# Kernel optimization log

Hardware: AMD Instinct MI355X
Metric: run time of the kernel (lower is better)

## Reference

```python
import jax, jax.numpy as jnp
import numpy as np

NEG_INF = -1e10
LEAKY_ALPHA = 0.2


def setup_inputs() -> dict:
    key = jax.random.key(0)
    k1, k2, k3, k4, k5 = jax.random.split(key, 5)
    N, F, H, D = 4096, 512, 8, 64
    X = jax.random.normal(k1, (N, F), dtype=jnp.float32)
    # dense 0/1 adjacency (float, as used by the mask formula)
    A = jax.random.randint(k2, (N, N), 0, 2).astype(jnp.float32)
    W = jax.random.normal(k3, (H, F, D), dtype=jnp.float32) * (1.0 / np.sqrt(F))
    b = jnp.zeros((H, D), dtype=jnp.float32)
    a_self = jax.random.normal(k4, (H, D), dtype=jnp.float32) * (1.0 / np.sqrt(D))
    a_neigh = jax.random.normal(k5, (H, D), dtype=jnp.float32) * (1.0 / np.sqrt(D))
    return {"X": X, "A": A, "W": W, "b": b, "a_self": a_self, "a_neigh": a_neigh}


def reference(X, A, W, b, a_self, a_neigh):
    # Multi-head dense GAT, heads vectorized. Dropout is identity (eval mode).
    # feats: [H, N, D]
    feats = jnp.einsum('nf,hfd->hnd', X, W)
    e_self = jnp.einsum('hnd,hd->hn', feats, a_self)    # [H, N]
    e_neigh = jnp.einsum('hnd,hd->hn', feats, a_neigh)  # [H, N]
    # outer-sum additive scores: [H, N, N]
    dense = e_self[:, :, None] + e_neigh[:, None, :]
    dense = jnp.where(dense >= 0, dense, LEAKY_ALPHA * dense)  # LeakyReLU(0.2)
    mask = NEG_INF * (1.0 - A)                                  # [N, N]
    dense = dense + mask[None, :, :]
    attn = jax.nn.softmax(dense, axis=-1)                       # [H, N, N]
    out = jnp.einsum('hnm,hmd->hnd', attn, feats) + b[:, None, :]
    # concat heads -> [N, H*D], then relu activation
    H, N, D = out.shape
    out = jnp.transpose(out, (1, 0, 2)).reshape(N, H * D)
    return jax.nn.relu(out)
```

## Files before the change

### kernel.cpp

```cpp
#include <hip/hip_runtime.h>
#include <hip/hip_fp16.h>
#include <stdint.h>


#define NODES 4096
#define FEAT  512
#define HEADS 8
#define DH    64
#define NT    (NODES / 64)

using half2v = __attribute__((ext_vector_type(2))) _Float16;
using half8  = __attribute__((ext_vector_type(8))) _Float16;
using f32x4  = __attribute__((ext_vector_type(4))) float;

__device__ __forceinline__ void gll16(const void* g, void* l) {
    __builtin_amdgcn_global_load_lds(
        (const __attribute__((address_space(1))) uint32_t*)g,
        (__attribute__((address_space(3))) uint32_t*)l, 16, 0, 0);
}

__device__ __forceinline__ uint32_t fenc(float f) {
    uint32_t u = __float_as_uint(f);
    return (u >> 31) ? ~u : (u | 0x80000000u);
}
__device__ __forceinline__ float fdec(uint32_t e) {
    uint32_t u = (e >> 31) ? (e & 0x7FFFFFFFu) : ~e;
    return __uint_as_float(u);
}

#define PACK_BLOCKS 16384
#define CAST_BLOCKS (NODES * FEAT / 4 / 256)
#define WT_BLOCKS   (HEADS * 8)

__global__ __launch_bounds__(256) void prep_kernel(
    const float* __restrict__ A, const float* __restrict__ X, const float* __restrict__ W,
    uint64_t* __restrict__ AbitsT, _Float16* __restrict__ Xh, _Float16* __restrict__ WT,
    uint32_t* __restrict__ enmax_u) {
    __shared__ float t[64][65];
    const int bx = blockIdx.x;
    if (bx < PACK_BLOCKS) {
        const int w    = threadIdx.x >> 6;
        const int lane = threadIdx.x & 63;
        const int v    = bx * 4 + w;
        const int wc   = v >> 10;
        const int rowb = (v & 1023) * 4;
        const float* ar = A + (size_t)wc * 64 + lane;
#pragma unroll
        for (int tt = 0; tt < 4; ++tt) {
            uint64_t m = __ballot(ar[(size_t)(rowb + tt) * NODES] != 0.0f);
            if (lane == 0) AbitsT[(size_t)wc * NODES + rowb + tt] = m;
        }
        return;
    }
    if (bx < PACK_BLOCKS + CAST_BLOCKS) {
        if (bx == PACK_BLOCKS && threadIdx.x < 16) enmax_u[threadIdx.x] = 0;
        int i = ((bx - PACK_BLOCKS) * 256 + threadIdx.x) * 4;
        f32x4 x = *(const f32x4*)(X + i);
        *(half2v*)(Xh + i)     = half2v{(_Float16)x[0], (_Float16)x[1]};
        *(half2v*)(Xh + i + 2) = half2v{(_Float16)x[2], (_Float16)x[3]};
        return;
    }
    const int b2 = bx - PACK_BLOCKS - CAST_BLOCKS;
    const int h  = b2 >> 3;
    const int ft = b2 & 7;
    const int r  = threadIdx.x >> 6;
    const int c  = threadIdx.x & 63;
#pragma unroll
    for (int r0 = 0; r0 < 64; r0 += 4)
        t[r0 + r][c] = W[((size_t)h * FEAT + ft * 64 + r0 + r) * DH + c];
    __syncthreads();
#pragma unroll
    for (int r0 = 0; r0 < 64; r0 += 4)
        WT[((size_t)h * DH + r0 + r) * FEAT + ft * 64 + c] = (_Float16)t[c][r0 + r];
}

__global__ __launch_bounds__(256) void feats_kernel(
    const _Float16* __restrict__ Xh, const _Float16* __restrict__ WT,
    const float* __restrict__ a_self, const float* __restrict__ a_neigh,
    _Float16* __restrict__ Vt, float* __restrict__ e_self,
    _Float16* __restrict__ u_tab, _Float16* __restrict__ v_tab,
    uint32_t* __restrict__ enmax_u) {
    const int h    = blockIdx.y;
    const int bx   = blockIdx.x;
    const int tid  = threadIdx.x;
    const int w    = tid >> 6;
    const int lane = tid & 63;
    const int l15  = lane & 15;
    const int g    = lane >> 4;
    const int n0   = bx * 64 + w * 16;

    f32x4 acc[4] = {};
    const _Float16* xb = Xh + (n0 + l15) * FEAT + g * 8;
    const _Float16* wb = WT + (h * DH + l15) * FEAT + g * 8;

#pragma unroll
    for (int kk = 0; kk < FEAT / 32; ++kk) {
        half8 b = *(const half8*)(xb + kk * 32);
#pragma unroll
        for (int mi = 0; mi < 4; ++mi) {
            half8 a = *(const half8*)(wb + mi * 16 * FEAT + kk * 32);
            acc[mi] = __builtin_amdgcn_mfma_f32_16x16x32_f16(a, b, acc[mi], 0, 0, 0);
        }
    }

    const int cc = w * 2 + (l15 >> 3);
    const int e  = l15 & 7;
    float ps = 0.f, pn = 0.f;
#pragma unroll
    for (int mi = 0; mi < 4; ++mi) {
#pragma unroll
        for (int r = 0; r < 4; ++r) {
            int d = mi * 16 + g * 4 + r;
            float v = acc[mi][r];
            Vt[((size_t)h * NT + bx) * 4096 + cc * 512 + d * 8 + e] = (_Float16)v;
            ps += v * a_self[h * DH + d];
            pn += v * a_neigh[h * DH + d];
        }
    }
    ps += __shfl_xor(ps, 16); ps += __shfl_xor(ps, 32);
    pn += __shfl_xor(pn, 16); pn += __shfl_xor(pn, 32);
    if (g == 0) {
        int n = n0 + l15;
        e_self[h * NODES + n] = ps;
        u_tab[h * NODES + n]  = (_Float16)__expf(pn);
        v_tab[h * NODES + n]  = (_Float16)__expf(0.2f * pn);
    }
    float mx = pn;
    mx = fmaxf(mx, __shfl_xor(mx, 1));
    mx = fmaxf(mx, __shfl_xor(mx, 2));
    mx = fmaxf(mx, __shfl_xor(mx, 4));
    mx = fmaxf(mx, __shfl_xor(mx, 8));
    if (lane == 0) atomicMax(enmax_u + h, fenc(mx));
}

__global__ __launch_bounds__(256, 4) void attn_kernel(
    const uint64_t* __restrict__ AbitsT, const _Float16* __restrict__ Vt,
    const float* __restrict__ e_self, const _Float16* __restrict__ u_tab,
    const _Float16* __restrict__ v_tab, const uint32_t* __restrict__ enmax_u,
    const float* __restrict__ bias, float* __restrict__ out) {
    __shared__ __align__(16) _Float16 Vlds[2][2][4096];
    float* redf = (float*)&Vlds[0][0][0];

    const int tid  = threadIdx.x;
    const int w    = tid >> 6;
    const int lane = tid & 63;
    const int l15  = lane & 15;
    const int g    = lane >> 4;
    const int g8   = g * 8;
    const int rh   = w & 1;
    const int jq   = w >> 1;
    const int h    = blockIdx.x & 7;
    const int i0   = (blockIdx.x >> 3) * 32;

    const float em = fdec(enmax_u[h]);
    const float es = e_self[h * NODES + i0 + rh * 16 + l15];
    const float t0 = es + em;
    const float M  = fmaxf(t0, 0.2f * t0);
    const _Float16 c1 = (_Float16)__expf(es - M);
    const _Float16 c2 = (_Float16)__expf(0.2f * es - M);
    const half2v c1h = half2v{c1, c1};
    const half2v c2h = half2v{c2, c2};

    const _Float16* ub  = u_tab + h * NODES + jq * 2048 + g8;
    const _Float16* vb  = v_tab + h * NODES + jq * 2048 + g8;
    const uint64_t* ab  = AbitsT + (size_t)(jq * 32) * NODES + i0 + rh * 16 + l15;
    const _Float16* vtb = Vt + ((size_t)h * NT + jq * 32) * 4096;

#define STAGE(s_, buf_) do {                                        \
        const _Float16* vs_ = vtb + (size_t)(s_) * 4096;            \
        _Float16* vd_ = &Vlds[jq][buf_][0];                         \
        _Pragma("unroll")                                           \
        for (int p_ = 0; p_ < 4; ++p_) {                            \
            const int c_ = rh * 256 + p_ * 64 + lane;               \
            gll16(vs_ + c_ * 8, vd_ + c_ * 8);                      \
        }                                                           \
    } while (0)

    f32x4 acc[4] = {};
    f32x4 asum = {};
    half8 ones;
#pragma unroll
    for (int e = 0; e < 8; ++e) ones[e] = (_Float16)1.0f;

    STAGE(0, 0);
    uint64_t wb_c = ab[0];
    half8 uf_c[2], vf_c[2];
#pragma unroll
    for (int kk = 0; kk < 2; ++kk) {
        uf_c[kk] = *(const half8*)(ub + kk * 32);
        vf_c[kk] = *(const half8*)(vb + kk * 32);
    }
    __syncthreads();

    for (int s = 0; s < 32; ++s) {
        const int buf = s & 1;
        STAGE(s + 1, buf ^ 1);
        uint64_t wb_n = ab[(size_t)(s + 1) * NODES];
        half8 uf_n[2], vf_n[2];
#pragma unroll
        for (int kk = 0; kk < 2; ++kk) {
            uf_n[kk] = *(const half8*)(ub + (s + 1) * 64 + kk * 32);
            vf_n[kk] = *(const half8*)(vb + (s + 1) * 64 + kk * 32);
        }

        const _Float16* vl = &Vlds[jq][buf][0];
#pragma unroll
        for (int kk = 0; kk < 2; ++kk) {
            const uint32_t b0 = ((uint32_t)(wb_c >> (kk * 32)) >> g8) & 0xFFu;
            half8 paf;
#pragma unroll
            for (int q = 0; q < 4; ++q) {
                half2v u2 = half2v{uf_c[kk][2 * q], uf_c[kk][2 * q + 1]};
                half2v v2 = half2v{vf_c[kk][2 * q], vf_c[kk][2 * q + 1]};
                half2v p2 = __builtin_elementwise_max(u2 * c1h, v2 * c2h);
                uint32_t mlo = (uint32_t)(-(int32_t)((b0 >> (2 * q)) & 1u));
                uint32_t mhi = (uint32_t)(-(int32_t)((b0 >> (2 * q + 1)) & 1u));
                uint32_t m = (mhi & 0xFFFF0000u) | (mlo & 0xFFFFu);
                p2 = __builtin_bit_cast(half2v, __builtin_bit_cast(uint32_t, p2) & m);
                paf[2 * q] = p2[0]; paf[2 * q + 1] = p2[1];
            }
            __builtin_amdgcn_s_setprio(1);
#pragma unroll
            for (int ni = 0; ni < 4; ++ni) {
                const half8 vfr = *(const half8*)(vl + (kk * 4 + g) * 512 + (ni * 16 + l15) * 8);
                acc[ni] = __builtin_amdgcn_mfma_f32_16x16x32_f16(paf, vfr, acc[ni], 0, 0, 0);
            }
            asum = __builtin_amdgcn_mfma_f32_16x16x32_f16(paf, ones, asum, 0, 0, 0);
            __builtin_amdgcn_s_setprio(0);
        }
        wb_c = wb_n;
#pragma unroll
        for (int kk = 0; kk < 2; ++kk) { uf_c[kk] = uf_n[kk]; vf_c[kk] = vf_n[kk]; }
        __syncthreads();
    }

    if (jq == 1) {
#pragma unroll
        for (int ni = 0; ni < 4; ++ni)
#pragma unroll
            for (int r = 0; r < 4; ++r)
                redf[(rh * 16 + g * 4 + r) * 68 + ni * 16 + l15] = acc[ni][r];
        if (l15 == 0) {
#pragma unroll
            for (int r = 0; r < 4; ++r)
                redf[2176 + rh * 16 + g * 4 + r] = asum[r];
        }
    }
    __syncthreads();
    if (jq == 0) {
        float invr[4];
#pragma unroll
        for (int r = 0; r < 4; ++r)
            invr[r] = 1.0f / (asum[r] + redf[2176 + rh * 16 + g * 4 + r]);
#pragma unroll
        for (int ni = 0; ni < 4; ++ni) {
            float bb = bias[h * DH + ni * 16 + l15];
#pragma unroll
            for (int r = 0; r < 4; ++r) {
                float v = (acc[ni][r] + redf[(rh * 16 + g * 4 + r) * 68 + ni * 16 + l15]) * invr[r] + bb;
                out[(size_t)(i0 + rh * 16 + g * 4 + r) * (HEADS * DH) + h * DH + ni * 16 + l15] =
                    fmaxf(v, 0.f);
            }
        }
    }
#undef STAGE
}

extern "C" void kernel_launch(void* const* d_in, const int* in_sizes, int n_in,
                              void* d_out, int out_size, void* d_ws, size_t ws_size,
                              hipStream_t stream) {
    const float* X       = (const float*)d_in[0];
    const float* A       = (const float*)d_in[1];
    const float* W       = (const float*)d_in[2];
    const float* b       = (const float*)d_in[3];
    const float* a_self  = (const float*)d_in[4];
    const float* a_neigh = (const float*)d_in[5];
    float* out = (float*)d_out;

    char* ws = (char*)d_ws;
    size_t off = 0;
    uint64_t* AbitsT = (uint64_t*)(ws + off); off += (size_t)64 * NODES * 8;
    _Float16* Xh     = (_Float16*)(ws + off); off += (size_t)NODES * FEAT * 2;
    _Float16* WT     = (_Float16*)(ws + off); off += (size_t)HEADS * DH * FEAT * 2;
    _Float16* Vt     = (_Float16*)(ws + off); off += (size_t)HEADS * DH * NODES * 2;
    float* e_self    = (float*)(ws + off);    off += (size_t)HEADS * NODES * 4;
    _Float16* u_tab  = (_Float16*)(ws + off); off += (size_t)HEADS * NODES * 2;
    _Float16* v_tab  = (_Float16*)(ws + off); off += (size_t)HEADS * NODES * 2;
    uint32_t* enmax_u = (uint32_t*)(ws + off); off += 64;

    prep_kernel<<<PACK_BLOCKS + CAST_BLOCKS + WT_BLOCKS, 256, 0, stream>>>(
        A, X, W, AbitsT, Xh, WT, enmax_u);
    feats_kernel<<<dim3(NODES / 64, HEADS), 256, 0, stream>>>(
        Xh, WT, a_self, a_neigh, Vt, e_self, u_tab, v_tab, enmax_u);
    attn_kernel<<<(NODES / 32) * HEADS, 256, 0, stream>>>(
        AbitsT, Vt, e_self, u_tab, v_tab, enmax_u, b, out);
}
```

Baseline: 108.9 us.

## Drop X fp16 cast pass, retile adjacency bitmask, split-K feats, relax attention barriers

Result: slower. 118.6 us (+8.9%).

```diff
diff --git a/kernel.cpp b/kernel.cpp
--- a/kernel.cpp
+++ b/kernel.cpp
@@ -28,39 +28,29 @@
     return __uint_as_float(u);
 }
 
-#define PACK_BLOCKS 16384
-#define CAST_BLOCKS (NODES * FEAT / 4 / 256)
+#define PACK_BLOCKS 1024
 #define WT_BLOCKS   (HEADS * 8)
 
 __global__ __launch_bounds__(256) void prep_kernel(
-    const float* __restrict__ A, const float* __restrict__ X, const float* __restrict__ W,
-    uint64_t* __restrict__ AbitsT, _Float16* __restrict__ Xh, _Float16* __restrict__ WT,
+    const float* __restrict__ A, const float* __restrict__ W,
+    uint64_t* __restrict__ Abits2, _Float16* __restrict__ WT,
     uint32_t* __restrict__ enmax_u) {
     __shared__ float t[64][65];
     const int bx = blockIdx.x;
     if (bx < PACK_BLOCKS) {
+        if (bx == 0 && threadIdx.x < 16) enmax_u[threadIdx.x] = 0;
         const int w    = threadIdx.x >> 6;
         const int lane = threadIdx.x & 63;
-        const int v    = bx * 4 + w;
-        const int wc   = v >> 10;
-        const int rowb = (v & 1023) * 4;
-        const float* ar = A + (size_t)wc * 64 + lane;
-#pragma unroll
-        for (int tt = 0; tt < 4; ++tt) {
-            uint64_t m = __ballot(ar[(size_t)(rowb + tt) * NODES] != 0.0f);
-            if (lane == 0) AbitsT[(size_t)wc * NODES + rowb + tt] = m;
+        const int row  = bx * 4 + w;
+        const float* ar = A + (size_t)row * NODES + lane;
+        uint64_t* dst = Abits2 + (size_t)(row >> 5) * 2048 + (row & 31);
+        for (int wc = 0; wc < 64; ++wc) {
+            uint64_t m = __ballot(ar[wc * 64] != 0.0f);
+            if (lane == 0) dst[wc * 32] = m;
         }
         return;
     }
-    if (bx < PACK_BLOCKS + CAST_BLOCKS) {
-        if (bx == PACK_BLOCKS && threadIdx.x < 16) enmax_u[threadIdx.x] = 0;
-        int i = ((bx - PACK_BLOCKS) * 256 + threadIdx.x) * 4;
-        f32x4 x = *(const f32x4*)(X + i);
-        *(half2v*)(Xh + i)     = half2v{(_Float16)x[0], (_Float16)x[1]};
-        *(half2v*)(Xh + i + 2) = half2v{(_Float16)x[2], (_Float16)x[3]};
-        return;
-    }
-    const int b2 = bx - PACK_BLOCKS - CAST_BLOCKS;
+    const int b2 = bx - PACK_BLOCKS;
     const int h  = b2 >> 3;
     const int ft = b2 & 7;
     const int r  = threadIdx.x >> 6;
@@ -74,12 +64,13 @@
         WT[((size_t)h * DH + r0 + r) * FEAT + ft * 64 + c] = (_Float16)t[c][r0 + r];
 }
 
-__global__ __launch_bounds__(256) void feats_kernel(
-    const _Float16* __restrict__ Xh, const _Float16* __restrict__ WT,
+__global__ __launch_bounds__(512) void feats_kernel(
+    const float* __restrict__ X, const _Float16* __restrict__ WT,
     const float* __restrict__ a_self, const float* __restrict__ a_neigh,
     _Float16* __restrict__ Vt, float* __restrict__ e_self,
     _Float16* __restrict__ u_tab, _Float16* __restrict__ v_tab,
     uint32_t* __restrict__ enmax_u) {
+    __shared__ float cmb[4][64][17];
     const int h    = blockIdx.y;
     const int bx   = blockIdx.x;
     const int tid  = threadIdx.x;
@@ -87,54 +78,71 @@
     const int lane = tid & 63;
     const int l15  = lane & 15;
     const int g    = lane >> 4;
-    const int n0   = bx * 64 + w * 16;
+    const int ns   = w & 3;
+    const int kh   = w >> 2;
+    const int n0   = bx * 64 + ns * 16;
 
     f32x4 acc[4] = {};
-    const _Float16* xb = Xh + (n0 + l15) * FEAT + g * 8;
+    const float* xb = X + (size_t)(n0 + l15) * FEAT + g * 8;
     const _Float16* wb = WT + (h * DH + l15) * FEAT + g * 8;
 
 #pragma unroll
-    for (int kk = 0; kk < FEAT / 32; ++kk) {
-        half8 b = *(const half8*)(xb + kk * 32);
+    for (int kk = 0; kk < 8; ++kk) {
+        const int k = (kh * 8 + kk) * 32;
+        f32x4 x0 = *(const f32x4*)(xb + k);
+        f32x4 x1 = *(const f32x4*)(xb + k + 4);
+        half8 b;
+#pragma unroll
+        for (int e = 0; e < 4; ++e) { b[e] = (_Float16)x0[e]; b[e + 4] = (_Float16)x1[e]; }
 #pragma unroll
         for (int mi = 0; mi < 4; ++mi) {
-            half8 a = *(const half8*)(wb + mi * 16 * FEAT + kk * 32);
+            half8 a = *(const half8*)(wb + mi * 16 * FEAT + k);
             acc[mi] = __builtin_amdgcn_mfma_f32_16x16x32_f16(a, b, acc[mi], 0, 0, 0);
         }
     }
 
-    const int cc = w * 2 + (l15 >> 3);
-    const int e  = l15 & 7;
-    float ps = 0.f, pn = 0.f;
-#pragma unroll
-    for (int mi = 0; mi < 4; ++mi) {
-#pragma unroll
-        for (int r = 0; r < 4; ++r) {
-            int d = mi * 16 + g * 4 + r;
-            float v = acc[mi][r];
-            Vt[((size_t)h * NT + bx) * 4096 + cc * 512 + d * 8 + e] = (_Float16)v;
-            ps += v * a_self[h * DH + d];
-            pn += v * a_neigh[h * DH + d];
-        }
-    }
-    ps += __shfl_xor(ps, 16); ps += __shfl_xor(ps, 32);
-    pn += __shfl_xor(pn, 16); pn += __shfl_xor(pn, 32);
-    if (g == 0) {
-        int n = n0 + l15;
-        e_self[h * NODES + n] = ps;
-        u_tab[h * NODES + n]  = (_Float16)__expf(pn);
-        v_tab[h * NODES + n]  = (_Float16)__expf(0.2f * pn);
-    }
-    float mx = pn;
-    mx = fmaxf(mx, __shfl_xor(mx, 1));
-    mx = fmaxf(mx, __shfl_xor(mx, 2));
-    mx = fmaxf(mx, __shfl_xor(mx, 4));
-    mx = fmaxf(mx, __shfl_xor(mx, 8));
-    if (lane == 0) atomicMax(enmax_u + h, fenc(mx));
+    if (kh == 1) {
+#pragma unroll
+        for (int mi = 0; mi < 4; ++mi)
+#pragma unroll
+            for (int r = 0; r < 4; ++r)
+                cmb[ns][mi * 16 + g * 4 + r][l15] = acc[mi][r];
+    }
+    __syncthreads();
+    if (kh == 0) {
+        const int cc = ns * 2 + (l15 >> 3);
+        const int e  = l15 & 7;
+        float ps = 0.f, pn = 0.f;
+#pragma unroll
+        for (int mi = 0; mi < 4; ++mi) {
+#pragma unroll
+            for (int r = 0; r < 4; ++r) {
+                int d = mi * 16 + g * 4 + r;
+                float v = acc[mi][r] + cmb[ns][d][l15];
+                Vt[((size_t)h * NT + bx) * 4096 + cc * 512 + d * 8 + e] = (_Float16)v;
+                ps += v * a_self[h * DH + d];
+                pn += v * a_neigh[h * DH + d];
+            }
+        }
+        ps += __shfl_xor(ps, 16); ps += __shfl_xor(ps, 32);
+        pn += __shfl_xor(pn, 16); pn += __shfl_xor(pn, 32);
+        if (g == 0) {
+            int n = n0 + l15;
+            e_self[h * NODES + n] = ps;
+            u_tab[h * NODES + n]  = (_Float16)__expf(pn);
+            v_tab[h * NODES + n]  = (_Float16)__expf(0.2f * pn);
+        }
+        float mx = pn;
+        mx = fmaxf(mx, __shfl_xor(mx, 1));
+        mx = fmaxf(mx, __shfl_xor(mx, 2));
+        mx = fmaxf(mx, __shfl_xor(mx, 4));
+        mx = fmaxf(mx, __shfl_xor(mx, 8));
+        if (lane == 0) atomicMax(enmax_u + h, fenc(mx));
+    }
 }
 
 __global__ __launch_bounds__(256, 4) void attn_kernel(
-    const uint64_t* __restrict__ AbitsT, const _Float16* __restrict__ Vt,
+    const uint64_t* __restrict__ Abits2, const _Float16* __restrict__ Vt,
     const float* __restrict__ e_self, const _Float16* __restrict__ u_tab,
     const _Float16* __restrict__ v_tab, const uint32_t* __restrict__ enmax_u,
     const float* __restrict__ bias, float* __restrict__ out) {
@@ -150,7 +158,8 @@
     const int rh   = w & 1;
     const int jq   = w >> 1;
     const int h    = blockIdx.x & 7;
-    const int i0   = (blockIdx.x >> 3) * 32;
+    const int itile = blockIdx.x >> 3;
+    const int i0   = itile * 32;
 
     const float em = fdec(enmax_u[h]);
     const float es = e_self[h * NODES + i0 + rh * 16 + l15];
@@ -163,7 +172,7 @@
 
     const _Float16* ub  = u_tab + h * NODES + jq * 2048 + g8;
     const _Float16* vb  = v_tab + h * NODES + jq * 2048 + g8;
-    const uint64_t* ab  = AbitsT + (size_t)(jq * 32) * NODES + i0 + rh * 16 + l15;
+    const uint64_t* ab2 = Abits2 + (size_t)itile * 2048 + (jq * 32) * 32 + rh * 16 + l15;
     const _Float16* vtb = Vt + ((size_t)h * NT + jq * 32) * 4096;
 
 #define STAGE(s_, buf_) do {                                        \
@@ -183,19 +192,23 @@
     for (int e = 0; e < 8; ++e) ones[e] = (_Float16)1.0f;
 
     STAGE(0, 0);
-    uint64_t wb_c = ab[0];
+    uint64_t wb_c = ab2[0];
     half8 uf_c[2], vf_c[2];
 #pragma unroll
     for (int kk = 0; kk < 2; ++kk) {
         uf_c[kk] = *(const half8*)(ub + kk * 32);
         vf_c[kk] = *(const half8*)(vb + kk * 32);
     }
-    __syncthreads();
-
+    asm volatile("s_waitcnt vmcnt(5)" ::: "memory");
+    __builtin_amdgcn_sched_barrier(0);
+    __builtin_amdgcn_s_barrier();
+    __builtin_amdgcn_sched_barrier(0);
+
+#pragma unroll 2
     for (int s = 0; s < 32; ++s) {
         const int buf = s & 1;
         STAGE(s + 1, buf ^ 1);
-        uint64_t wb_n = ab[(size_t)(s + 1) * NODES];
+        uint64_t wb_n = ab2[(size_t)(s + 1) * 32];
         half8 uf_n[2], vf_n[2];
 #pragma unroll
         for (int kk = 0; kk < 2; ++kk) {
@@ -213,8 +226,8 @@
                 half2v u2 = half2v{uf_c[kk][2 * q], uf_c[kk][2 * q + 1]};
                 half2v v2 = half2v{vf_c[kk][2 * q], vf_c[kk][2 * q + 1]};
                 half2v p2 = __builtin_elementwise_max(u2 * c1h, v2 * c2h);
-                uint32_t mlo = (uint32_t)(-(int32_t)((b0 >> (2 * q)) & 1u));
-                uint32_t mhi = (uint32_t)(-(int32_t)((b0 >> (2 * q + 1)) & 1u));
+                uint32_t mlo = (uint32_t)((int32_t)(b0 << (31 - 2 * q)) >> 31);
+                uint32_t mhi = (uint32_t)((int32_t)(b0 << (30 - 2 * q)) >> 31);
                 uint32_t m = (mhi & 0xFFFF0000u) | (mlo & 0xFFFFu);
                 p2 = __builtin_bit_cast(half2v, __builtin_bit_cast(uint32_t, p2) & m);
                 paf[2 * q] = p2[0]; paf[2 * q + 1] = p2[1];
@@ -231,7 +244,11 @@
         wb_c = wb_n;
 #pragma unroll
         for (int kk = 0; kk < 2; ++kk) { uf_c[kk] = uf_n[kk]; vf_c[kk] = vf_n[kk]; }
-        __syncthreads();
+
+        asm volatile("s_waitcnt vmcnt(5)" ::: "memory");
+        __builtin_amdgcn_sched_barrier(0);
+        __builtin_amdgcn_s_barrier();
+        __builtin_amdgcn_sched_barrier(0);
     }
 
     if (jq == 1) {
@@ -279,7 +296,7 @@
 
     char* ws = (char*)d_ws;
     size_t off = 0;
-    uint64_t* AbitsT = (uint64_t*)(ws + off); off += (size_t)64 * NODES * 8;
+    uint64_t* Abits2 = (uint64_t*)(ws + off); off += (size_t)128 * 2048 * 8;
     _Float16* Xh     = (_Float16*)(ws + off); off += (size_t)NODES * FEAT * 2;
     _Float16* WT     = (_Float16*)(ws + off); off += (size_t)HEADS * DH * FEAT * 2;
     _Float16* Vt     = (_Float16*)(ws + off); off += (size_t)HEADS * DH * NODES * 2;
@@ -287,11 +304,11 @@
     _Float16* u_tab  = (_Float16*)(ws + off); off += (size_t)HEADS * NODES * 2;
     _Float16* v_tab  = (_Float16*)(ws + off); off += (size_t)HEADS * NODES * 2;
     uint32_t* enmax_u = (uint32_t*)(ws + off); off += 64;
-
-    prep_kernel<<<PACK_BLOCKS + CAST_BLOCKS + WT_BLOCKS, 256, 0, stream>>>(
-        A, X, W, AbitsT, Xh, WT, enmax_u);
-    feats_kernel<<<dim3(NODES / 64, HEADS), 256, 0, stream>>>(
-        Xh, WT, a_self, a_neigh, Vt, e_self, u_tab, v_tab, enmax_u);
+    (void)Xh;
+
+    prep_kernel<<<PACK_BLOCKS + WT_BLOCKS, 256, 0, stream>>>(A, W, Abits2, WT, enmax_u);
+    feats_kernel<<<dim3(NODES / 64, HEADS), 512, 0, stream>>>(
+        X, WT, a_self, a_neigh, Vt, e_self, u_tab, v_tab, enmax_u);
     attn_kernel<<<(NODES / 32) * HEADS, 256, 0, stream>>>(
-        AbitsT, Vt, e_self, u_tab, v_tab, enmax_u, b, out);
-}
+        Abits2, Vt, e_self, u_tab, v_tab, enmax_u, b, out);
+}
```
